# Optimization experiments

Measured on AMD Instinct MI355X. Metric: run time of the kernel, lower is better.

## Reference

```python
import jax, jax.numpy as jnp
import numpy as np

N, C, E, H = 50000, 128, 1_600_000, 32
JITTER = 1e-20


def _lin(k, fan_in, fan_out):
    return jax.random.normal(k, (fan_in, fan_out), jnp.float32) / np.sqrt(fan_in)


def setup_inputs() -> dict:
    key = jax.random.key(0)
    ks = jax.random.split(key, 20)
    x = jax.random.normal(ks[0], (N, C), jnp.float32)
    edge_index = jax.random.randint(ks[1], (2, E), 0, N, dtype=jnp.int64)
    inp = {"x": x, "edge_index": edge_index}
    # actor params
    inp["aW"] = _lin(ks[2], C, C); inp["ab"] = jnp.zeros((C,), jnp.float32)
    inp["a1W"] = _lin(ks[3], C, H); inp["a1b"] = jnp.zeros((H,), jnp.float32)
    inp["a2W"] = _lin(ks[4], H, H); inp["a2b"] = jnp.zeros((H,), jnp.float32)
    inp["a3W"] = _lin(ks[5], H, 2); inp["a3b"] = jnp.zeros((2,), jnp.float32)
    # critic params
    inp["cW"] = _lin(ks[6], C, C); inp["cb"] = jnp.zeros((C,), jnp.float32)
    inp["c1W"] = _lin(ks[7], C, H); inp["c1b"] = jnp.zeros((H,), jnp.float32)
    inp["c2W"] = _lin(ks[8], H, H); inp["c2b"] = jnp.zeros((H,), jnp.float32)
    inp["c3W"] = _lin(ks[9], H, 2); inp["c3b"] = jnp.zeros((2,), jnp.float32)
    return inp


def gcn_conv(x, src, dst, W, b):
    """Standard PyG GCNConv: add self-loops, symmetric degree norm, X@W, scatter-add, +bias."""
    n = x.shape[0]
    loop = jnp.arange(n)
    s = jnp.concatenate([src, loop])  # [E+N]
    d = jnp.concatenate([dst, loop])
    deg = jax.ops.segment_sum(jnp.ones_like(d, jnp.float32), d, num_segments=n)
    dinv = jnp.where(deg > 0, jax.lax.rsqrt(deg), 0.0)
    norm = dinv[s] * dinv[d]                     # [E+N]
    h = x @ W                                    # [N, C]
    agg = jax.ops.segment_sum(h[s] * norm[:, None], d, num_segments=n)
    return agg + b


def reference(x, edge_index, aW, ab, a1W, a1b, a2W, a2b, a3W, a3b,
              cW, cb, c1W, c1b, c2W, c2b, c3W, c3b):
    src, dst = edge_index[0], edge_index[1]
    # actor
    h = jax.nn.relu(gcn_conv(x, src, dst, aW, ab)) + x
    h = jax.nn.relu(h @ a1W + a1b)
    h = jax.nn.relu(h @ a2W + a2b)
    a = h @ a3W + a3b                            # [N, 2]
    concentration = jax.nn.softplus(a[:, 0]) + JITTER
    p = jax.nn.softplus(a[:, 1])
    action2_probs = p / jnp.sum(p)
    # critic
    hc = jax.nn.relu(gcn_conv(x, src, dst, cW, cb)) + x
    hc = jnp.sum(hc, axis=0)                     # [C]
    hc = jax.nn.relu(hc @ c1W + c1b)
    hc = jax.nn.relu(hc @ c2W + c2b)
    value = hc @ c3W + c3b                       # [2]
    return (concentration, value, action2_probs)
```

## Files before the change

### kernel.cpp

```cpp
#include <hip/hip_runtime.h>
#include <hip/hip_bf16.h>
#include <hip/hip_fp16.h>
#include <math.h>

#define C 128
#define BCAP 12288

using half8x = __attribute__((ext_vector_type(8))) _Float16;
using half4x = __attribute__((ext_vector_type(4))) _Float16;
using f32x4  = __attribute__((ext_vector_type(4))) float;

__device__ inline float4 h4_to_f4(uint2 u) {
    __half2 p0 = *(__half2*)&u.x;
    __half2 p1 = *(__half2*)&u.y;
    float2 f0 = __half22float2(p0), f1 = __half22float2(p1);
    return make_float4(f0.x, f0.y, f1.x, f1.y);
}

__device__ inline float softplusf(float v) {
    return (v > 20.f) ? v : log1pf(expf(v));
}

__global__ __launch_bounds__(256) void initk(unsigned* gcur, float* colsum, float* pSum) {
    int t = threadIdx.x;
    gcur[t] = 0u;
    if (t < 128) colsum[t] = 0.f;
    if (t == 128) pSum[0] = 0.f;
}

__global__ __launch_bounds__(256) void wtk(const float* __restrict__ aW, const float* __restrict__ cW,
                                           const float* __restrict__ a1W,
                                           __half* __restrict__ wt, __half* __restrict__ a1wt) {
    int idx = blockIdx.x * 256 + threadIdx.x;
    if (idx < 32768) {
        int y = idx >> 14, r = idx & 16383;
        int k = r >> 7, n = r & 127;
        const float* W = y ? cW : aW;
        wt[((size_t)y << 14) + n * 128 + k] = __float2half(W[k * 128 + n]);
    } else if (idx < 36864) {
        int r = idx - 32768;
        int k = r >> 5, n = r & 31;
        a1wt[n * 128 + k] = __float2half(a1W[k * 32 + n]);
    }
}

__global__ __launch_bounds__(256) void bink(const int* __restrict__ ei,
                                            unsigned* __restrict__ gcur,
                                            unsigned* __restrict__ gstage,
                                            int E, int NBKT) {
    __shared__ unsigned raw[6400];
    __shared__ unsigned image[6400];
    __shared__ unsigned cnt[256];
    __shared__ unsigned pref[256];
    __shared__ unsigned cur[256];
    __shared__ unsigned gb[256];
    int t = threadIdx.x, b = blockIdx.x;
    int elo = (int)((long long)b * E / 256);
    int ehi = (int)((long long)(b + 1) * E / 256);
    int n = ehi - elo;

    for (int i = t; i < n; i += 256) {
        int d = __builtin_nontemporal_load(ei + E + elo + i);
        int s = __builtin_nontemporal_load(ei + elo + i);
        raw[i] = (unsigned)s | ((unsigned)(d & 255) << 16) | ((unsigned)(d >> 8) << 24);
    }
    cnt[t] = 0u; cur[t] = 0u;
    __syncthreads();
    for (int i = t; i < n; i += 256) atomicAdd(&cnt[raw[i] >> 24], 1u);
    __syncthreads();
    pref[t] = cnt[t];
    __syncthreads();
    for (int off = 1; off < 256; off <<= 1) {
        unsigned add = (t >= off) ? pref[t - off] : 0u;
        __syncthreads();
        pref[t] += add;
        __syncthreads();
    }
    gb[t] = (t < NBKT && cnt[t]) ? atomicAdd(&gcur[t], cnt[t]) : 0u;
    __syncthreads();
    for (int i = t; i < n; i += 256) {
        unsigned v = raw[i];
        unsigned B = v >> 24;
        unsigned pos = (pref[B] - cnt[B]) + atomicAdd(&cur[B], 1u);
        image[pos] = v & 0xFFFFFFu;
    }
    __syncthreads();
    int wv = t >> 6, lane = t & 63;
    for (int B = wv; B < NBKT; B += 4) {
        unsigned c = cnt[B];
        if (!c) continue;
        unsigned eb = pref[B] - c;
        unsigned gbase = gb[B];
        unsigned c2 = (gbase < BCAP) ? ((c < BCAP - gbase) ? c : BCAP - gbase) : 0u;
        for (unsigned i = lane; i < c2; i += 64)
            gstage[(size_t)B * BCAP + gbase + i] = image[eb + i];
    }
}

__global__ void bktscank(const unsigned* __restrict__ gcur, unsigned* __restrict__ bktbase, int NBKT) {
    __shared__ unsigned tmp[256];
    int t = threadIdx.x;
    unsigned g = (t < NBKT) ? gcur[t] : 0u;
    unsigned v = (g < BCAP) ? g : BCAP;
    tmp[t] = v;
    __syncthreads();
    for (int off = 1; off < 256; off <<= 1) {
        unsigned add = (t >= off) ? tmp[t - off] : 0u;
        __syncthreads();
        tmp[t] += add;
        __syncthreads();
    }
    if (t < NBKT) bktbase[t] = tmp[t] - v;
}

__global__ __launch_bounds__(256) void placek(const unsigned* __restrict__ gstage,
                                              const unsigned* __restrict__ gcur,
                                              const unsigned* __restrict__ bktbase,
                                              int* __restrict__ rowptr, float* __restrict__ dinv,
                                              int* __restrict__ col, int N, int NBKT) {
    __shared__ unsigned image[BCAP];
    __shared__ unsigned cnt[256];
    __shared__ unsigned pref[256];
    __shared__ unsigned cur[256];
    int B = blockIdx.x, t = threadIdx.x;
    unsigned g = gcur[B];
    unsigned m = (g < BCAP) ? g : BCAP;
    unsigned base = bktbase[B];
    const unsigned* st = gstage + (size_t)B * BCAP;

    cnt[t] = 0u; cur[t] = 0u;
    __syncthreads();
    for (unsigned i = t; i < m; i += 256) atomicAdd(&cnt[(st[i] >> 16) & 255u], 1u);
    __syncthreads();
    pref[t] = cnt[t];
    __syncthreads();
    for (int off = 1; off < 256; off <<= 1) {
        unsigned add = (t >= off) ? pref[t - off] : 0u;
        __syncthreads();
        pref[t] += add;
        __syncthreads();
    }
    int d = B * 256 + t;
    if (d < N) {
        rowptr[d] = (int)(base + pref[t] - cnt[t]);
        dinv[d] = rsqrtf((float)(cnt[t] + 1u));
    }
    if (B == NBKT - 1 && t == 0) rowptr[N] = (int)(base + m);
    for (unsigned i = t; i < m; i += 256) {
        unsigned v = st[i];
        unsigned dl = (v >> 16) & 255u;
        unsigned pos = (pref[dl] - cnt[dl]) + atomicAdd(&cur[dl], 1u);
        image[pos] = v & 0xFFFFu;
    }
    __syncthreads();
    for (unsigned i = t; i < m; i += 256) col[base + i] = (int)image[i];
}

__global__ __launch_bounds__(256) void xhk(const float* __restrict__ x, const float* __restrict__ dinv,
                                           __half* __restrict__ xh, __half* __restrict__ x16, int N) {
    int i = blockIdx.x * 256 + threadIdx.x;
    if (i >= N * 64) return;
    int node = i >> 6, fp = (i & 63) * 2;
    float w = dinv[node];
    float2 f = *(const float2*)&x[(size_t)node * C + fp];
    __half2 h = __floats2half2_rn(f.x * w, f.y * w);
    __half2 hx = __floats2half2_rn(f.x, f.y);
    *(unsigned*)&xh[(size_t)node * C + fp] = *(unsigned*)&h;
    *(unsigned*)&x16[(size_t)node * C + fp] = *(unsigned*)&hx;
}

__global__ __launch_bounds__(256) void gatherk(const int* __restrict__ col,
                                               const int* __restrict__ rowptr,
                                               const __half* __restrict__ xh,
                                               const float* __restrict__ dinv,
                                               __half* __restrict__ gg, int N) {
    __shared__ int snb[4][64];
    int t = threadIdx.x;
    int wid = t >> 6, lane = t & 63;
    int d = blockIdx.x * 4 + wid;
    if (d >= N) return;
    int beg = rowptr[d], end = rowptr[d + 1];
    int half = lane >> 5, sub = lane & 31;
    int f = sub * 4;

    float a0 = 0.f, a1 = 0.f, a2 = 0.f, a3 = 0.f;

    for (int c = beg; c < end; c += 64) {
        if (c + lane < end) snb[wid][lane] = col[c + lane];
        int n = end - c; if (n > 64) n = 64;
        int j = 0;
        for (; j + 3 < n; j += 4) {
            size_t i0 = (size_t)snb[wid][j + half] * C + f;
            size_t i1 = (size_t)snb[wid][j + 2 + half] * C + f;
            float4 v0 = h4_to_f4(*(const uint2*)&xh[i0]);
            float4 v1 = h4_to_f4(*(const uint2*)&xh[i1]);
            a0 += v0.x + v1.x;
            a1 += v0.y + v1.y;
            a2 += v0.z + v1.z;
            a3 += v0.w + v1.w;
        }
        for (; j < n; j += 2) {
            if (j + half < n) {
                float4 v = h4_to_f4(*(const uint2*)&xh[(size_t)snb[wid][j + half] * C + f]);
                a0 += v.x; a1 += v.y; a2 += v.z; a3 += v.w;
            }
        }
    }
    a0 += __shfl_xor(a0, 32, 64);
    a1 += __shfl_xor(a1, 32, 64);
    a2 += __shfl_xor(a2, 32, 64);
    a3 += __shfl_xor(a3, 32, 64);

    if (half == 0) {
        float4 s4 = h4_to_f4(*(const uint2*)&xh[(size_t)d * C + f]);
        float dv = dinv[d];
        __half2 h0 = __floats2half2_rn((a0 + s4.x) * dv, (a1 + s4.y) * dv);
        __half2 h1 = __floats2half2_rn((a2 + s4.z) * dv, (a3 + s4.w) * dv);
        uint2 u; u.x = *(unsigned*)&h0; u.y = *(unsigned*)&h1;
        *(uint2*)&gg[(size_t)d * C + f] = u;
    }
}

__global__ __launch_bounds__(256) void gemm2k(const __half* __restrict__ gg,
                                              const __half* __restrict__ wt,
                                              const __half* __restrict__ a1wt,
                                              const float* __restrict__ ab, const float* __restrict__ cb,
                                              const __half* __restrict__ x16,
                                              const float* __restrict__ a1b,
                                              const float* __restrict__ a2W, const float* __restrict__ a2b,
                                              const float* __restrict__ a3W, const float* __restrict__ a3b,
                                              float* __restrict__ scratch,
                                              float* __restrict__ out, float* __restrict__ pSum, int N) {
    __shared__ char As[32768];
    __shared__ char Aux[13312];
    const bool actor = (blockIdx.y == 0);
    const float* bias = actor ? ab : cb;
    const __half* W = wt + (actor ? 0 : 16384);
    const int row0 = blockIdx.x * 128;
    const int t = threadIdx.x;

    _Float16* w2t = (_Float16*)Aux;
    _Float16* h1b = (_Float16*)(Aux + 2560);
    float* w3s    = (float*)(Aux + 12800);

#pragma unroll
    for (int i = 0; i < 8; ++i) {
        int c = t + i * 256;
        int row = c >> 4, cb16 = (c & 15) * 16;
        int grow = row0 + row;
        uint4 u = make_uint4(0u, 0u, 0u, 0u);
        if (grow < N) u = *(const uint4*)&gg[(size_t)grow * C + (c & 15) * 8];
        *(uint4*)(As + row * 256 + (cb16 ^ ((row & 7) << 4))) = u;
    }
    if (actor) {
#pragma unroll
        for (int i = 0; i < 4; ++i) {
            int idx = t + i * 256;
            int k = idx >> 5, n = idx & 31;
            w2t[n * 40 + k] = (_Float16)a2W[idx];
        }
        if (t < 64) w3s[t] = a3W[t];
    }
    __syncthreads();

    int wv = t >> 6, l = t & 63;
    int lm = l & 15, lk = l >> 4;
    int koffB = lk * 16;
    int koffH = lk * 8;

    half8x af[2][4];
#pragma unroll
    for (int r = 0; r < 2; ++r) {
        int row = wv * 32 + r * 16 + lm;
        const char* rp = As + row * 256;
        int sw = (row & 7) << 4;
#pragma unroll
        for (int kc = 0; kc < 4; ++kc)
            af[r][kc] = *(const half8x*)(rp + ((kc * 64 + koffB) ^ sw));
    }

    float csum[8];
#pragma unroll
    for (int nc = 0; nc < 8; ++nc) csum[nc] = 0.f;

#pragma unroll
    for (int nc = 0; nc < 8; ++nc) {
        int n = nc * 16 + lm;
        const __half* wp = W + n * 128;
        half8x bf[4];
#pragma unroll
        for (int kc = 0; kc < 4; ++kc)
            bf[kc] = *(const half8x*)(wp + kc * 32 + koffH);
        float bsv = bias[n];
#pragma unroll
        for (int r = 0; r < 2; ++r) {
            f32x4 acc = {0.f, 0.f, 0.f, 0.f};
#pragma unroll
            for (int kc = 0; kc < 4; ++kc)
                acc = __builtin_amdgcn_mfma_f32_16x16x32_f16(af[r][kc], bf[kc], acc, 0, 0, 0);
            int grl0 = wv * 32 + r * 16 + lk * 4;
#pragma unroll
            for (int j = 0; j < 4; ++j) {
                int rowL = grl0 + j;
                int grow = row0 + rowL;
                float v = 0.f;
                if (grow < N) v = fmaxf(acc[j] + bsv, 0.f) + __half2float(x16[(size_t)grow * C + n]);
                if (actor) {
                    *(_Float16*)(As + rowL * 256 + ((n * 2) ^ ((rowL & 7) << 4))) = (_Float16)v;
                } else {
                    csum[nc] += v;
                }
            }
        }
    }
    __syncthreads();

    if (actor) {
#pragma unroll
        for (int rt = 0; rt < 2; ++rt) {
            int rowA = wv * 32 + rt * 16 + lm;
            const char* rp = As + rowA * 256;
            int swA = (rowA & 7) << 4;
            half8x a1f[4];
#pragma unroll
            for (int kc = 0; kc < 4; ++kc)
                a1f[kc] = *(const half8x*)(rp + ((kc * 64 + koffB) ^ swA));
#pragma unroll
            for (int ct = 0; ct < 2; ++ct) {
                int n = ct * 16 + lm;
                const __half* ap = a1wt + n * 128;
                f32x4 acc1 = {0.f, 0.f, 0.f, 0.f};
#pragma unroll
                for (int kc = 0; kc < 4; ++kc) {
                    half8x bq = *(const half8x*)(ap + kc * 32 + koffH);
                    acc1 = __builtin_amdgcn_mfma_f32_16x16x32_f16(a1f[kc], bq, acc1, 0, 0, 0);
                }
                float bv = a1b[n];
#pragma unroll
                for (int j = 0; j < 4; ++j)
                    h1b[(wv * 32 + rt * 16 + lk * 4 + j) * 40 + n] = (_Float16)fmaxf(acc1[j] + bv, 0.f);
            }
        }

        float wave_psum = 0.f;
        float b30 = a3b[0], b31 = a3b[1];
#pragma unroll
        for (int rt = 0; rt < 2; ++rt) {
            int rowH = wv * 32 + rt * 16 + lm;
            half4x alo = *(const half4x*)(h1b + rowH * 40 + koffH);
            half4x ahi = *(const half4x*)(h1b + rowH * 40 + koffH + 4);
            half8x a2f = __builtin_shufflevector(alo, ahi, 0, 1, 2, 3, 4, 5, 6, 7);
            float p0[4] = {0.f, 0.f, 0.f, 0.f}, p1[4] = {0.f, 0.f, 0.f, 0.f};
#pragma unroll
            for (int ct = 0; ct < 2; ++ct) {
                int n = ct * 16 + lm;
                half4x blo = *(const half4x*)(w2t + n * 40 + koffH);
                half4x bhi = *(const half4x*)(w2t + n * 40 + koffH + 4);
                half8x b2f = __builtin_shufflevector(blo, bhi, 0, 1, 2, 3, 4, 5, 6, 7);
                f32x4 acc2 = {0.f, 0.f, 0.f, 0.f};
                acc2 = __builtin_amdgcn_mfma_f32_16x16x32_f16(a2f, b2f, acc2, 0, 0, 0);
                float bv = a2b[n];
                float w30 = w3s[n * 2], w31 = w3s[n * 2 + 1];
#pragma unroll
                for (int j = 0; j < 4; ++j) {
                    float h2v = fmaxf(acc2[j] + bv, 0.f);
                    p0[j] += h2v * w30;
                    p1[j] += h2v * w31;
                }
            }
#pragma unroll
            for (int j = 0; j < 4; ++j) {
                float q0 = p0[j], q1 = p1[j];
                q0 += __shfl_xor(q0, 1, 64); q0 += __shfl_xor(q0, 2, 64);
                q0 += __shfl_xor(q0, 4, 64); q0 += __shfl_xor(q0, 8, 64);
                q1 += __shfl_xor(q1, 1, 64); q1 += __shfl_xor(q1, 2, 64);
                q1 += __shfl_xor(q1, 4, 64); q1 += __shfl_xor(q1, 8, 64);
                if (lm == 0) {
                    int node = row0 + wv * 32 + rt * 16 + lk * 4 + j;
                    if (node < N) {
                        float s0 = softplusf(q0 + b30);
                        float s1 = softplusf(q1 + b31);
                        out[node] = s0 + 1e-20f;
                        out[(size_t)N + 2 + node] = s1;
                        wave_psum += s1;
                    }
                }
            }
        }
        wave_psum += __shfl_xor(wave_psum, 16, 64);
        wave_psum += __shfl_xor(wave_psum, 32, 64);
        if (l == 0) atomicAdd(pSum, wave_psum);
    } else {
        float* scol = (float*)Aux;
#pragma unroll
        for (int nc = 0; nc < 8; ++nc) {
            float v = csum[nc];
            v += __shfl_xor(v, 16, 64);
            v += __shfl_xor(v, 32, 64);
            if (lk == 0) scol[wv * 128 + nc * 16 + lm] = v;
        }
        __syncthreads();
        if (t < 128)
            scratch[(size_t)blockIdx.x * 128 + t] = scol[t] + scol[128 + t] + scol[256 + t] + scol[384 + t];
    }
}

__global__ __launch_bounds__(128) void csredk(const float* __restrict__ scratch, float* __restrict__ colsum, int nblk) {
    int t = threadIdx.x;
    float s = 0.f;
    for (int b = blockIdx.x; b < nblk; b += gridDim.x)
        s += scratch[(size_t)b * 128 + t];
    atomicAdd(&colsum[t], s);
}

__global__ void critick(const float* __restrict__ colsum,
                        const float* __restrict__ c1W, const float* __restrict__ c1b,
                        const float* __restrict__ c2W, const float* __restrict__ c2b,
                        const float* __restrict__ c3W, const float* __restrict__ c3b,
                        float* __restrict__ out, int N) {
    __shared__ float s1[32], s2[32];
    int t = threadIdx.x;
    if (t < 32) {
        float acc = c1b[t];
        for (int k = 0; k < 128; ++k) acc += colsum[k] * c1W[k * 32 + t];
        s1[t] = fmaxf(acc, 0.f);
    }
    __syncthreads();
    if (t < 32) {
        float acc = c2b[t];
        for (int k = 0; k < 32; ++k) acc += s1[k] * c2W[k * 32 + t];
        s2[t] = fmaxf(acc, 0.f);
    }
    __syncthreads();
    if (t < 2) {
        float acc = c3b[t];
        for (int k = 0; k < 32; ++k) acc += s2[k] * c3W[k * 2 + t];
        out[(size_t)N + t] = acc;
    }
}

__global__ __launch_bounds__(256) void normk(float* __restrict__ out, const float* __restrict__ pSum, int N) {
    int i = blockIdx.x * 256 + threadIdx.x;
    if (i < N) out[(size_t)N + 2 + i] /= pSum[0];
}

extern "C" void kernel_launch(void* const* d_in, const int* in_sizes, int n_in,
                              void* d_out, int out_size, void* d_ws, size_t ws_size,
                              hipStream_t stream) {
    const float* x   = (const float*)d_in[0];
    const int* ei    = (const int*)d_in[1];
    const float* aW  = (const float*)d_in[2];
    const float* ab  = (const float*)d_in[3];
    const float* a1W = (const float*)d_in[4];
    const float* a1b = (const float*)d_in[5];
    const float* a2W = (const float*)d_in[6];
    const float* a2b = (const float*)d_in[7];
    const float* a3W = (const float*)d_in[8];
    const float* a3b = (const float*)d_in[9];
    const float* cW  = (const float*)d_in[10];
    const float* cb  = (const float*)d_in[11];
    const float* c1W = (const float*)d_in[12];
    const float* c1b = (const float*)d_in[13];
    const float* c2W = (const float*)d_in[14];
    const float* c2b = (const float*)d_in[15];
    const float* c3W = (const float*)d_in[16];
    const float* c3b = (const float*)d_in[17];

    const int N = in_sizes[0] / C;
    const int E = in_sizes[1] / 2;
    const int NBKT = (N + 255) / 256;
    const int nblkx = (N + 127) / 128;
    float* out = (float*)d_out;

    char* ws = (char*)d_ws;
    size_t off = 0;
    auto alloc = [&](size_t bytes) {
        size_t o = off;
        off = (off + bytes + 255) & ~(size_t)255;
        return (void*)(ws + o);
    };
    unsigned* gcur    = (unsigned*)alloc(256 * 4);
    unsigned* bktbase = (unsigned*)alloc(256 * 4);
    unsigned* gstage  = (unsigned*)alloc((size_t)NBKT * BCAP * 4);
    int* rowptr       = (int*)alloc((size_t)(N + 1) * 4);
    float* dinv       = (float*)alloc((size_t)N * 4);
    int* colidx       = (int*)alloc((size_t)E * 4);
    __half* xh        = (__half*)alloc((size_t)N * C * 2);
    __half* x16       = (__half*)alloc((size_t)N * C * 2);
    __half* gg        = (__half*)alloc((size_t)N * C * 2);
    __half* wt        = (__half*)alloc(2 * 16384 * 2);
    __half* a1wt      = (__half*)alloc(4096 * 2);
    float* scratch    = (float*)alloc((size_t)nblkx * 128 * 4);
    float* colsum     = (float*)alloc(128 * 4);
    float* pSum       = (float*)alloc(4);

    initk<<<1, 256, 0, stream>>>(gcur, colsum, pSum);
    wtk<<<144, 256, 0, stream>>>(aW, cW, a1W, wt, a1wt);
    bink<<<256, 256, 0, stream>>>(ei, gcur, gstage, E, NBKT);
    bktscank<<<1, 256, 0, stream>>>(gcur, bktbase, NBKT);
    placek<<<NBKT, 256, 0, stream>>>(gstage, gcur, bktbase, rowptr, dinv, colidx, N, NBKT);
    xhk<<<(N * 64 + 255) / 256, 256, 0, stream>>>(x, dinv, xh, x16, N);
    gatherk<<<(N + 3) / 4, 256, 0, stream>>>(colidx, rowptr, xh, dinv, gg, N);
    gemm2k<<<dim3(nblkx, 2), 256, 0, stream>>>(gg, wt, a1wt, ab, cb, x16,
                                               a1b, a2W, a2b, a3W, a3b,
                                               scratch, out, pSum, N);
    csredk<<<8, 128, 0, stream>>>(scratch, colsum, nblkx);
    critick<<<1, 64, 0, stream>>>(colsum, c1W, c1b, c2W, c2b, c3W, c3b, out, N);
    normk<<<(N + 255) / 256, 256, 0, stream>>>(out, pSum, N);
}
```

Measured before the change: 204.2 us.

## Halve gemm2k row tile and transpose MFMA operands for vectorized epilogue

The fused GEMM/MLP kernel now handles 64 rows per block instead of 128, one 16-row tile per wave, and uses about half the shared memory. The MFMA operands are swapped so each lane holds four consecutive output features. That allows vectorized bias loads, x16 residual loads and half4 stores to LDS, replacing scalar per-element accesses. The critic column sums are reduced with shuffles inside the loop and the per-node softplus reduction is simplified. The aim is more blocks, better occupancy and fewer scalar memory operations, at the cost of twice as many partial-sum rows for csredk to reduce and weight fragments being reloaded per block.

```diff
diff --git a/kernel.cpp b/kernel.cpp
--- a/kernel.cpp
+++ b/kernel.cpp
@@ -231,20 +231,21 @@
                                               const float* __restrict__ a3W, const float* __restrict__ a3b,
                                               float* __restrict__ scratch,
                                               float* __restrict__ out, float* __restrict__ pSum, int N) {
-    __shared__ char As[32768];
-    __shared__ char Aux[13312];
+    __shared__ char As[16384];
+    __shared__ char Aux[8192];
     const bool actor = (blockIdx.y == 0);
     const float* bias = actor ? ab : cb;
     const __half* W = wt + (actor ? 0 : 16384);
-    const int row0 = blockIdx.x * 128;
+    const int row0 = blockIdx.x * 64;
     const int t = threadIdx.x;
 
     _Float16* w2t = (_Float16*)Aux;
     _Float16* h1b = (_Float16*)(Aux + 2560);
-    float* w3s    = (float*)(Aux + 12800);
-
-#pragma unroll
-    for (int i = 0; i < 8; ++i) {
+    float* w3s    = (float*)(Aux + 7680);
+    float* scol   = (float*)Aux;
+
+#pragma unroll
+    for (int i = 0; i < 4; ++i) {
         int c = t + i * 256;
         int row = c >> 4, cb16 = (c & 15) * 16;
         int grow = row0 + row;
@@ -268,138 +269,121 @@
     int koffB = lk * 16;
     int koffH = lk * 8;
 
-    half8x af[2][4];
-#pragma unroll
-    for (int r = 0; r < 2; ++r) {
-        int row = wv * 32 + r * 16 + lm;
-        const char* rp = As + row * 256;
-        int sw = (row & 7) << 4;
+    const int rowA = wv * 16 + lm;
+    const int grow = row0 + rowA;
+    const bool valid = grow < N;
+    const int sw = (rowA & 7) << 4;
+
+    half8x af[4];
+    {
+        const char* rp = As + rowA * 256;
 #pragma unroll
         for (int kc = 0; kc < 4; ++kc)
-            af[r][kc] = *(const half8x*)(rp + ((kc * 64 + koffB) ^ sw));
-    }
-
-    float csum[8];
-#pragma unroll
-    for (int nc = 0; nc < 8; ++nc) csum[nc] = 0.f;
+            af[kc] = *(const half8x*)(rp + ((kc * 64 + koffB) ^ sw));
+    }
 
 #pragma unroll
     for (int nc = 0; nc < 8; ++nc) {
-        int n = nc * 16 + lm;
-        const __half* wp = W + n * 128;
+        const __half* wp = W + (nc * 16 + lm) * 128;
         half8x bf[4];
 #pragma unroll
         for (int kc = 0; kc < 4; ++kc)
             bf[kc] = *(const half8x*)(wp + kc * 32 + koffH);
-        float bsv = bias[n];
-#pragma unroll
-        for (int r = 0; r < 2; ++r) {
-            f32x4 acc = {0.f, 0.f, 0.f, 0.f};
+        f32x4 acc = {0.f, 0.f, 0.f, 0.f};
+#pragma unroll
+        for (int kc = 0; kc < 4; ++kc)
+            acc = __builtin_amdgcn_mfma_f32_16x16x32_f16(bf[kc], af[kc], acc, 0, 0, 0);
+        float4 bv = *(const float4*)&bias[nc * 16 + lk * 4];
+        half4x xq = {};
+        if (valid) xq = *(const half4x*)&x16[(size_t)grow * C + nc * 16 + lk * 4];
+        float v0 = valid ? fmaxf(acc[0] + bv.x, 0.f) + (float)xq[0] : 0.f;
+        float v1 = valid ? fmaxf(acc[1] + bv.y, 0.f) + (float)xq[1] : 0.f;
+        float v2 = valid ? fmaxf(acc[2] + bv.z, 0.f) + (float)xq[2] : 0.f;
+        float v3 = valid ? fmaxf(acc[3] + bv.w, 0.f) + (float)xq[3] : 0.f;
+        if (actor) {
+            half4x hv = { (_Float16)v0, (_Float16)v1, (_Float16)v2, (_Float16)v3 };
+            *(half4x*)(As + rowA * 256 + ((nc * 32 + lk * 8) ^ sw)) = hv;
+        } else {
+            v0 += __shfl_xor(v0, 1, 64); v0 += __shfl_xor(v0, 2, 64);
+            v0 += __shfl_xor(v0, 4, 64); v0 += __shfl_xor(v0, 8, 64);
+            v1 += __shfl_xor(v1, 1, 64); v1 += __shfl_xor(v1, 2, 64);
+            v1 += __shfl_xor(v1, 4, 64); v1 += __shfl_xor(v1, 8, 64);
+            v2 += __shfl_xor(v2, 1, 64); v2 += __shfl_xor(v2, 2, 64);
+            v2 += __shfl_xor(v2, 4, 64); v2 += __shfl_xor(v2, 8, 64);
+            v3 += __shfl_xor(v3, 1, 64); v3 += __shfl_xor(v3, 2, 64);
+            v3 += __shfl_xor(v3, 4, 64); v3 += __shfl_xor(v3, 8, 64);
+            if (lm == 0) {
+                float4 st = make_float4(v0, v1, v2, v3);
+                *(float4*)&scol[wv * 128 + nc * 16 + lk * 4] = st;
+            }
+        }
+    }
+    __syncthreads();
+
+    if (actor) {
+        half8x a1f[4];
+        {
+            const char* rp = As + rowA * 256;
 #pragma unroll
             for (int kc = 0; kc < 4; ++kc)
-                acc = __builtin_amdgcn_mfma_f32_16x16x32_f16(af[r][kc], bf[kc], acc, 0, 0, 0);
-            int grl0 = wv * 32 + r * 16 + lk * 4;
+                a1f[kc] = *(const half8x*)(rp + ((kc * 64 + koffB) ^ sw));
+        }
+#pragma unroll
+        for (int ct = 0; ct < 2; ++ct) {
+            const __half* ap = a1wt + (ct * 16 + lm) * 128;
+            f32x4 acc1 = {0.f, 0.f, 0.f, 0.f};
+#pragma unroll
+            for (int kc = 0; kc < 4; ++kc) {
+                half8x bq = *(const half8x*)(ap + kc * 32 + koffH);
+                acc1 = __builtin_amdgcn_mfma_f32_16x16x32_f16(bq, a1f[kc], acc1, 0, 0, 0);
+            }
+            float4 b1v = *(const float4*)&a1b[ct * 16 + lk * 4];
+            half4x h = { (_Float16)fmaxf(acc1[0] + b1v.x, 0.f),
+                         (_Float16)fmaxf(acc1[1] + b1v.y, 0.f),
+                         (_Float16)fmaxf(acc1[2] + b1v.z, 0.f),
+                         (_Float16)fmaxf(acc1[3] + b1v.w, 0.f) };
+            *(half4x*)((char*)h1b + rowA * 80 + ct * 32 + lk * 8) = h;
+        }
+
+        half4x alo = *(const half4x*)((char*)h1b + rowA * 80 + lk * 16);
+        half4x ahi = *(const half4x*)((char*)h1b + rowA * 80 + lk * 16 + 8);
+        half8x a2f = __builtin_shufflevector(alo, ahi, 0, 1, 2, 3, 4, 5, 6, 7);
+        float p0 = 0.f, p1 = 0.f;
+#pragma unroll
+        for (int ct = 0; ct < 2; ++ct) {
+            half4x blo = *(const half4x*)((char*)w2t + (ct * 16 + lm) * 80 + lk * 16);
+            half4x bhi = *(const half4x*)((char*)w2t + (ct * 16 + lm) * 80 + lk * 16 + 8);
+            half8x b2f = __builtin_shufflevector(blo, bhi, 0, 1, 2, 3, 4, 5, 6, 7);
+            f32x4 acc2 = {0.f, 0.f, 0.f, 0.f};
+            acc2 = __builtin_amdgcn_mfma_f32_16x16x32_f16(b2f, a2f, acc2, 0, 0, 0);
+            float4 b2v = *(const float4*)&a2b[ct * 16 + lk * 4];
 #pragma unroll
             for (int j = 0; j < 4; ++j) {
-                int rowL = grl0 + j;
-                int grow = row0 + rowL;
-                float v = 0.f;
-                if (grow < N) v = fmaxf(acc[j] + bsv, 0.f) + __half2float(x16[(size_t)grow * C + n]);
-                if (actor) {
-                    *(_Float16*)(As + rowL * 256 + ((n * 2) ^ ((rowL & 7) << 4))) = (_Float16)v;
-                } else {
-                    csum[nc] += v;
-                }
+                int f = ct * 16 + lk * 4 + j;
+                float h2v = fmaxf(acc2[j] + (&b2v.x)[j], 0.f);
+                float2 w3 = *(const float2*)&w3s[f * 2];
+                p0 += h2v * w3.x;
+                p1 += h2v * w3.y;
             }
         }
-    }
-    __syncthreads();
-
-    if (actor) {
-#pragma unroll
-        for (int rt = 0; rt < 2; ++rt) {
-            int rowA = wv * 32 + rt * 16 + lm;
-            const char* rp = As + rowA * 256;
-            int swA = (rowA & 7) << 4;
-            half8x a1f[4];
-#pragma unroll
-            for (int kc = 0; kc < 4; ++kc)
-                a1f[kc] = *(const half8x*)(rp + ((kc * 64 + koffB) ^ swA));
-#pragma unroll
-            for (int ct = 0; ct < 2; ++ct) {
-                int n = ct * 16 + lm;
-                const __half* ap = a1wt + n * 128;
-                f32x4 acc1 = {0.f, 0.f, 0.f, 0.f};
-#pragma unroll
-                for (int kc = 0; kc < 4; ++kc) {
-                    half8x bq = *(const half8x*)(ap + kc * 32 + koffH);
-                    acc1 = __builtin_amdgcn_mfma_f32_16x16x32_f16(a1f[kc], bq, acc1, 0, 0, 0);
-                }
-                float bv = a1b[n];
-#pragma unroll
-                for (int j = 0; j < 4; ++j)
-                    h1b[(wv * 32 + rt * 16 + lk * 4 + j) * 40 + n] = (_Float16)fmaxf(acc1[j] + bv, 0.f);
-            }
-        }
-
+        p0 += __shfl_xor(p0, 16, 64); p0 += __shfl_xor(p0, 32, 64);
+        p1 += __shfl_xor(p1, 16, 64); p1 += __shfl_xor(p1, 32, 64);
         float wave_psum = 0.f;
-        float b30 = a3b[0], b31 = a3b[1];
-#pragma unroll
-        for (int rt = 0; rt < 2; ++rt) {
-            int rowH = wv * 32 + rt * 16 + lm;
-            half4x alo = *(const half4x*)(h1b + rowH * 40 + koffH);
-            half4x ahi = *(const half4x*)(h1b + rowH * 40 + koffH + 4);
-            half8x a2f = __builtin_shufflevector(alo, ahi, 0, 1, 2, 3, 4, 5, 6, 7);
-            float p0[4] = {0.f, 0.f, 0.f, 0.f}, p1[4] = {0.f, 0.f, 0.f, 0.f};
-#pragma unroll
-            for (int ct = 0; ct < 2; ++ct) {
-                int n = ct * 16 + lm;
-                half4x blo = *(const half4x*)(w2t + n * 40 + koffH);
-                half4x bhi = *(const half4x*)(w2t + n * 40 + koffH + 4);
-                half8x b2f = __builtin_shufflevector(blo, bhi, 0, 1, 2, 3, 4, 5, 6, 7);
-                f32x4 acc2 = {0.f, 0.f, 0.f, 0.f};
-                acc2 = __builtin_amdgcn_mfma_f32_16x16x32_f16(a2f, b2f, acc2, 0, 0, 0);
-                float bv = a2b[n];
-                float w30 = w3s[n * 2], w31 = w3s[n * 2 + 1];
-#pragma unroll
-                for (int j = 0; j < 4; ++j) {
-                    float h2v = fmaxf(acc2[j] + bv, 0.f);
-                    p0[j] += h2v * w30;
-                    p1[j] += h2v * w31;
-                }
-            }
-#pragma unroll
-            for (int j = 0; j < 4; ++j) {
-                float q0 = p0[j], q1 = p1[j];
-                q0 += __shfl_xor(q0, 1, 64); q0 += __shfl_xor(q0, 2, 64);
-                q0 += __shfl_xor(q0, 4, 64); q0 += __shfl_xor(q0, 8, 64);
-                q1 += __shfl_xor(q1, 1, 64); q1 += __shfl_xor(q1, 2, 64);
-                q1 += __shfl_xor(q1, 4, 64); q1 += __shfl_xor(q1, 8, 64);
-                if (lm == 0) {
-                    int node = row0 + wv * 32 + rt * 16 + lk * 4 + j;
-                    if (node < N) {
-                        float s0 = softplusf(q0 + b30);
-                        float s1 = softplusf(q1 + b31);
-                        out[node] = s0 + 1e-20f;
-                        out[(size_t)N + 2 + node] = s1;
-                        wave_psum += s1;
-                    }
-                }
-            }
-        }
+        if (lk == 0 && valid) {
+            float s0 = softplusf(p0 + a3b[0]);
+            float s1 = softplusf(p1 + a3b[1]);
+            out[grow] = s0 + 1e-20f;
+            out[(size_t)N + 2 + grow] = s1;
+            wave_psum = s1;
+        }
+        wave_psum += __shfl_xor(wave_psum, 1, 64);
+        wave_psum += __shfl_xor(wave_psum, 2, 64);
+        wave_psum += __shfl_xor(wave_psum, 4, 64);
+        wave_psum += __shfl_xor(wave_psum, 8, 64);
         wave_psum += __shfl_xor(wave_psum, 16, 64);
         wave_psum += __shfl_xor(wave_psum, 32, 64);
         if (l == 0) atomicAdd(pSum, wave_psum);
     } else {
-        float* scol = (float*)Aux;
-#pragma unroll
-        for (int nc = 0; nc < 8; ++nc) {
-            float v = csum[nc];
-            v += __shfl_xor(v, 16, 64);
-            v += __shfl_xor(v, 32, 64);
-            if (lk == 0) scol[wv * 128 + nc * 16 + lm] = v;
-        }
-        __syncthreads();
         if (t < 128)
             scratch[(size_t)blockIdx.x * 128 + t] = scol[t] + scol[128 + t] + scol[256 + t] + scol[384 + t];
     }
@@ -469,7 +453,7 @@
     const int N = in_sizes[0] / C;
     const int E = in_sizes[1] / 2;
     const int NBKT = (N + 255) / 256;
-    const int nblkx = (N + 127) / 128;
+    const int nblk64 = (N + 63) / 64;
     float* out = (float*)d_out;
 
     char* ws = (char*)d_ws;
@@ -490,7 +474,7 @@
     __half* gg        = (__half*)alloc((size_t)N * C * 2);
     __half* wt        = (__half*)alloc(2 * 16384 * 2);
     __half* a1wt      = (__half*)alloc(4096 * 2);
-    float* scratch    = (float*)alloc((size_t)nblkx * 128 * 4);
+    float* scratch    = (float*)alloc((size_t)nblk64 * 128 * 4);
     float* colsum     = (float*)alloc(128 * 4);
     float* pSum       = (float*)alloc(4);
 
@@ -501,10 +485,10 @@
     placek<<<NBKT, 256, 0, stream>>>(gstage, gcur, bktbase, rowptr, dinv, colidx, N, NBKT);
     xhk<<<(N * 64 + 255) / 256, 256, 0, stream>>>(x, dinv, xh, x16, N);
     gatherk<<<(N + 3) / 4, 256, 0, stream>>>(colidx, rowptr, xh, dinv, gg, N);
-    gemm2k<<<dim3(nblkx, 2), 256, 0, stream>>>(gg, wt, a1wt, ab, cb, x16,
-                                               a1b, a2W, a2b, a3W, a3b,
-                                               scratch, out, pSum, N);
-    csredk<<<8, 128, 0, stream>>>(scratch, colsum, nblkx);
+    gemm2k<<<dim3(nblk64, 2), 256, 0, stream>>>(gg, wt, a1wt, ab, cb, x16,
+                                                a1b, a2W, a2b, a3W, a3b,
+                                                scratch, out, pSum, N);
+    csredk<<<8, 128, 0, stream>>>(scratch, colsum, nblk64);
     critick<<<1, 64, 0, stream>>>(colsum, c1W, c1b, c2W, c2b, c3W, c3b, out, N);
     normk<<<(N + 255) / 256, 256, 0, stream>>>(out, pSum, N);
 }
```

Result: slower. 236.5 us (+15.8%).
